# Kernel tuning notes

Measured on AMD Instinct MI355X. Metric: run time of the kernel, lower is better.

## Reference

```python
import jax, jax.numpy as jnp
import numpy as np

B, S, HID = 2, 4096, 1024
NH, HD = 16, 64
R = 2  # dilation_rate


def setup_inputs() -> dict:
    key = jax.random.key(0)
    ks = jax.random.split(key, 6)
    sc = 0.02
    return {
        "hidden_states": jax.random.normal(ks[0], (B, S, HID), jnp.float32),
        "Wq": jax.random.normal(ks[1], (HID, HID), jnp.float32) * sc,
        "Wk": jax.random.normal(ks[2], (HID, HID), jnp.float32) * sc,
        "Wv": jax.random.normal(ks[3], (HID, HID), jnp.float32) * sc,
        "Wo": jax.random.normal(ks[4], (HID, HID), jnp.float32) * sc,
        "bo": jnp.zeros((HID,), jnp.float32),
    }


def reference(hidden_states, Wq, Wk, Wv, Wo, bo):
    bsz, q_len, _ = hidden_states.shape
    # projections (torch Linear: y = x @ W.T)
    q = jnp.einsum('bsh,oh->bso', hidden_states, Wq).reshape(bsz, q_len, NH, HD).transpose(0, 2, 1, 3)
    k = jnp.einsum('bsh,oh->bso', hidden_states, Wk).reshape(bsz, q_len, NH, HD).transpose(0, 2, 1, 3)
    v = jnp.einsum('bsh,oh->bso', hidden_states, Wv).reshape(bsz, q_len, NH, HD).transpose(0, 2, 1, 3)
    # strided dilation gather (indices 0, R, 2R, ...)
    q = q[:, :, ::R, :]
    k = k[:, :, ::R, :]
    v = v[:, :, ::R, :]
    sd = q.shape[2]  # dilated length
    # SDPA with is_causal=True over the dilated subsequence
    scores = jnp.einsum('bhqd,bhkd->bhqk', q, k) / np.sqrt(HD).astype(np.float32)
    causal = jnp.tril(jnp.ones((sd, sd), bool))
    scores = jnp.where(causal, scores, jnp.finfo(scores.dtype).min)
    probs = jax.nn.softmax(scores, axis=-1)
    attn = jnp.einsum('bhqk,bhkd->bhqd', probs, v)  # [B, H, sd, HD]
    attn = attn.transpose(0, 2, 1, 3).reshape(bsz, sd, HID)
    # scatter back into zero-initialized full-length tensor
    full = jnp.zeros((bsz, q_len, HID), attn.dtype).at[:, ::R, :].set(attn)
    return jnp.einsum('bsh,oh->bso', full, Wo) + bo
```

## Files before the change

### kernel.cpp

```cpp
#include <hip/hip_runtime.h>
#include <cstdint>

typedef unsigned short u16;
typedef unsigned int u32;
typedef __attribute__((ext_vector_type(8))) short short8;
typedef __attribute__((ext_vector_type(4))) float f32x4;
typedef __attribute__((ext_vector_type(4))) unsigned short u16x4;

#define S_ 4096
#define SD 2048

__device__ __forceinline__ u16 f2bf(float f) {
  union { float f; u32 u; } v; v.f = f;
  u32 r = v.u + 0x7fffu + ((v.u >> 16) & 1u);
  return (u16)(r >> 16);
}
__device__ __forceinline__ float bf2f(u16 x) {
  union { u32 u; float f; } v; v.u = ((u32)x) << 16; return v.f;
}
#if __has_builtin(__builtin_amdgcn_cvt_pk_bf16_f32)
__device__ __forceinline__ u32 pkbf(float a, float b) {
  auto r = __builtin_amdgcn_cvt_pk_bf16_f32(a, b);
  u32 o; __builtin_memcpy(&o, &r, 4); return o;
}
#else
__device__ __forceinline__ u32 pkbf(float a, float b) {
  union { float f; u32 u; } ua, ub; ua.f = a; ub.f = b;
  return __builtin_amdgcn_perm(ub.u + 0x8000u, ua.u + 0x8000u, 0x07060302u);
}
#endif
__device__ __forceinline__ f32x4 mfma16(short8 a, short8 b, f32x4 c) {
  return __builtin_amdgcn_mfma_f32_16x16x32_bf16(a, b, c, 0, 0, 0);
}
__device__ __forceinline__ void async16(const void* g, void* l) {
  __builtin_amdgcn_global_load_lds((__attribute__((address_space(1))) void*)g,
                                   (__attribute__((address_space(3))) void*)l,
                                   16, 0, 0);
}

__global__ __launch_bounds__(256) void cast_all(const float* __restrict__ hs,
                                                const float* __restrict__ Wq,
                                                const float* __restrict__ Wk,
                                                const float* __restrict__ Wv,
                                                const float* __restrict__ Wo,
                                                u16* __restrict__ dstW,
                                                u16* __restrict__ dstX) {
  int bid = blockIdx.x;
  if (bid < 4096) {
    int gid = bid * 256 + threadIdx.x;
    int wsel = gid >> 18;
    int off  = (gid & 262143) * 4;
    const float* src = (wsel == 0) ? Wq : (wsel == 1) ? Wk : (wsel == 2) ? Wv : Wo;
    float scl = (wsel == 0) ? 0.18033688f : 1.0f;
    f32x4 v = *(const f32x4*)(src + off);
    u16x4 o; o.x = f2bf(v.x * scl); o.y = f2bf(v.y * scl);
    o.z = f2bf(v.z * scl); o.w = f2bf(v.w * scl);
    *(u16x4*)(dstW + (size_t)wsel * 1048576 + off) = o;
  } else {
    int gid = (bid - 4096) * 256 + threadIdx.x;
    int e = gid * 4;
    int m = e >> 10, col = e & 1023;
    int b = m >> 11, sm = m & 2047;
    const float* src = hs + ((size_t)(b * S_ + 2 * sm) << 10) + col;
    f32x4 v = *(const f32x4*)src;
    u16x4 o; o.x = f2bf(v.x); o.y = f2bf(v.y); o.z = f2bf(v.z); o.w = f2bf(v.w);
    *(u16x4*)(dstX + ((size_t)m << 10) + col) = o;
  }
}

template<int MODE>
__device__ __forceinline__ void gemm_body128_t(const u16* __restrict__ A,
                                               const u16* __restrict__ B,
                                               u16* __restrict__ C,
                                               int bm, int bn, char* lA, char* lB) {
  const int tid = threadIdx.x, lane = tid & 63, w = tid >> 6;
  const int quad = lane >> 4, l15 = lane & 15;
  const int wm = (w & 1) * 64, wn = (w >> 1) * 64;
  f32x4 acc[4][4] = {};

  auto stage = [&](int buf, int k0) {
#pragma unroll
    for (int i = 0; i < 2; i++) {
      int p = i * 256 + tid;
      int row = p >> 2, cp = p & 3;
      int c = cp ^ ((row ^ (row >> 2)) & 3);
      async16(A + (size_t)(bm + row) * 1024 + k0 + c * 8,
              lA + buf * 8192 + i * 4096 + w * 1024);
      async16(B + (size_t)(bn + row) * 1024 + k0 + c * 8,
              lB + buf * 8192 + i * 4096 + w * 1024);
    }
  };

  stage(0, 0);
#pragma unroll 1
  for (int kt = 0; kt < 32; kt++) {
    __syncthreads();
    if (kt + 1 < 32) stage((kt + 1) & 1, (kt + 1) * 32);
    const char* A_ = lA + (kt & 1) * 8192;
    const char* B_ = lB + (kt & 1) * 8192;
    short8 af[4], bf[4];
#pragma unroll
    for (int mi = 0; mi < 4; mi++) {
      int row = wm + mi * 16 + l15;
      af[mi] = *(const short8*)(A_ + (row * 4 + (quad ^ ((row ^ (row >> 2)) & 3))) * 16);
    }
#pragma unroll
    for (int ni = 0; ni < 4; ni++) {
      int row = wn + ni * 16 + l15;
      bf[ni] = *(const short8*)(B_ + (row * 4 + (quad ^ ((row ^ (row >> 2)) & 3))) * 16);
    }
#pragma unroll
    for (int mi = 0; mi < 4; mi++)
#pragma unroll
      for (int ni = 0; ni < 4; ni++)
        acc[mi][ni] = mfma16(af[mi], bf[ni], acc[mi][ni]);
  }

#pragma unroll
  for (int mi = 0; mi < 4; mi++)
#pragma unroll
    for (int ni = 0; ni < 4; ni++) {
      int m0 = bm + wm + mi * 16 + quad * 4;
      int n = bn + wn + ni * 16 + l15;
      size_t base;
      if (MODE == 0) {
        base = (size_t)m0 * 1024 + n;
      } else if (MODE == 1) {
        int bb = m0 >> 11, t = m0 & 2047, kb = t >> 6, key0 = t & 63;
        int d = n - 1024;
        int hh = d >> 6, dd = d & 63, ch = dd >> 3, e = dd & 7;
        base = ((size_t)(((bb * 16 + hh) * 32 + kb)) << 12)
             + (key0 >> 4) * 1024 + (ch >> 2) * 512 + (ch & 3) * 128
             + (key0 & 15) * 8 + e;
      } else {
        int hh = m0 >> 6, d0 = m0 & 63;
        int bb = n >> 11, t = n & 2047, kb = t >> 6, kk = t & 63;
        int kh = (kk & 32) | (((kk >> 2) & 3) << 3) | (((kk >> 4) & 1) << 2) | (kk & 3);
        int ch = kh >> 3, e = kh & 7;
        base = ((size_t)(((bb * 16 + hh) * 32 + kb)) << 12)
             + (d0 >> 4) * 1024 + (ch >> 2) * 512 + (ch & 3) * 128
             + (d0 & 15) * 8 + e;
      }
#pragma unroll
      for (int r = 0; r < 4; r++) {
        size_t off = (MODE == 0) ? base + (size_t)r * 1024 : base + (size_t)r * 8;
        C[off] = f2bf(acc[mi][ni][r]);
      }
    }
}

__global__ __launch_bounds__(256) void qkv_gemm(const u16* __restrict__ X,
                                                const u16* __restrict__ Wbf,
                                                u16* __restrict__ Qb,
                                                u16* __restrict__ Kp,
                                                u16* __restrict__ Vp) {
  __shared__ __align__(16) char lA[16384];
  __shared__ __align__(16) char lB[16384];
  int bid = blockIdx.x;
  if (bid < 512) {
    int bm = (bid >> 4) * 128, bn = (bid & 15) * 128;
    if (bn < 1024) gemm_body128_t<0>(X, Wbf, Qb, bm, bn, lA, lB);
    else           gemm_body128_t<1>(X, Wbf, Kp, bm, bn, lA, lB);
  } else {
    int b2 = bid - 512;
    gemm_body128_t<2>(Wbf + 2 * 1048576, X, Vp, (b2 >> 5) * 128, (b2 & 31) * 128, lA, lB);
  }
}

__global__ __launch_bounds__(256) void oproj(const u16* __restrict__ A,
                                             const u16* __restrict__ B,
                                             const float* __restrict__ bo,
                                             float* __restrict__ out) {
  __shared__ __align__(16) char lA[8192];
  __shared__ __align__(16) char lB[16384];
  const int tid = threadIdx.x, lane = tid & 63, w = tid >> 6;
  const int quad = lane >> 4, l15 = lane & 15;
  const int bm = blockIdx.y * 64, bn = blockIdx.x * 128;
  const int wm = (w & 1) * 32, wn = (w >> 1) * 64;
  f32x4 acc[2][4] = {};

  auto stage = [&](int buf, int k0) {
    {
      int row = tid >> 2, cp = tid & 3;
      int c = cp ^ ((row ^ (row >> 2)) & 3);
      async16(A + (size_t)(bm + row) * 1024 + k0 + c * 8, lA + buf * 4096 + w * 1024);
    }
#pragma unroll
    for (int i = 0; i < 2; i++) {
      int p = i * 256 + tid;
      int row = p >> 2, cp = p & 3;
      int c = cp ^ ((row ^ (row >> 2)) & 3);
      async16(B + (size_t)(bn + row) * 1024 + k0 + c * 8, lB + buf * 8192 + i * 4096 + w * 1024);
    }
  };

  stage(0, 0);
#pragma unroll 1
  for (int kt = 0; kt < 32; kt++) {
    __syncthreads();
    if (kt + 1 < 32) stage((kt + 1) & 1, (kt + 1) * 32);
    const char* A_ = lA + (kt & 1) * 4096;
    const char* B_ = lB + (kt & 1) * 8192;
    short8 af[2], bf[4];
#pragma unroll
    for (int mi = 0; mi < 2; mi++) {
      int row = wm + mi * 16 + l15;
      af[mi] = *(const short8*)(A_ + (row * 4 + (quad ^ ((row ^ (row >> 2)) & 3))) * 16);
    }
#pragma unroll
    for (int ni = 0; ni < 4; ni++) {
      int row = wn + ni * 16 + l15;
      bf[ni] = *(const short8*)(B_ + (row * 4 + (quad ^ ((row ^ (row >> 2)) & 3))) * 16);
    }
#pragma unroll
    for (int mi = 0; mi < 2; mi++)
#pragma unroll
      for (int ni = 0; ni < 4; ni++)
        acc[mi][ni] = mfma16(af[mi], bf[ni], acc[mi][ni]);
  }
#pragma unroll
  for (int mi = 0; mi < 2; mi++)
#pragma unroll
    for (int ni = 0; ni < 4; ni++) {
      int n = bn + wn + ni * 16 + l15;
      float bias = bo[n];
#pragma unroll
      for (int r = 0; r < 4; r++) {
        int m = bm + wm + mi * 16 + quad * 4 + r;
        int bb = m >> 11, sm = m & 2047;
        size_t grow = ((size_t)(bb * S_ + 2 * sm)) << 10;
        out[grow + n] = acc[mi][ni][r] + bias;
        out[grow + 1024 + n] = bias;
      }
    }
}

__global__ __launch_bounds__(256, 3) void attn11(const u16* __restrict__ Qb,
                                                 const u16* __restrict__ Kp,
                                                 const u16* __restrict__ Vp,
                                                 u16* __restrict__ O,
                                                 float* __restrict__ Op0,
                                                 u16* __restrict__ Op1,
                                                 float* __restrict__ lp) {
  const int tid = threadIdx.x, lane = tid & 63, w = tid >> 6;
  const int quad = lane >> 4, l15 = lane & 15;
  const int h = blockIdx.x, b = blockIdx.y;
  const int z = (int)blockIdx.z;
  int qt, chunk, c0, c1;
  if (z < 16) {
    qt = 15 - (z >> 1); chunk = z & 1;
    if (chunk == 0) { c0 = 0; c1 = qt; } else { c0 = qt + 1; c1 = 2 * qt + 1; }
  } else {
    qt = 23 - z; chunk = 0; c0 = 0; c1 = 2 * qt + 1;
  }
  const bool par = (z < 16);
  const int qb = qt * 128 + w * 32;
  const int qt2 = 2 * qt;

  short8 qf[2][2];
#pragma unroll
  for (int n = 0; n < 2; n++) {
    const u16* qp = Qb + (size_t)(b * SD + qb + n * 16 + l15) * 1024 + h * 64 + quad * 8;
    qf[n][0] = *(const short8*)qp;
    qf[n][1] = *(const short8*)(qp + 32);
  }

  const size_t bh = (size_t)(b * 16 + h) * 32;
  f32x4 oacc[2][4] = {};
  f32x4 l4v[2] = {};
  const f32x4 zf = {};

#pragma unroll 1
  for (int kt = c0; kt <= c1; kt++) {
    const u16* K_ = Kp + ((bh + kt) << 12);
    const u16* V_ = Vp + ((bh + kt) << 12);
    const bool diag = (kt >= qt2);

    short8 kf[4][2];
#pragma unroll
    for (int m = 0; m < 4; m++) {
      kf[m][0] = *(const short8*)(K_ + m * 1024 + lane * 8);
      kf[m][1] = *(const short8*)(K_ + m * 1024 + 512 + lane * 8);
    }
    f32x4 s[4][2];
#pragma unroll
    for (int m = 0; m < 4; m++)
#pragma unroll
      for (int n = 0; n < 2; n++) {
        f32x4 a = mfma16(kf[m][0], qf[n][0], zf);
        s[m][n] = mfma16(kf[m][1], qf[n][1], a);
      }
    short8 vf[4][2];
#pragma unroll
    for (int m = 0; m < 4; m++) {
      vf[m][0] = *(const short8*)(V_ + m * 1024 + lane * 8);
      vf[m][1] = *(const short8*)(V_ + m * 1024 + 512 + lane * 8);
    }
    u32 pw[2][8];
#pragma unroll
    for (int m = 0; m < 4; m++)
#pragma unroll
      for (int n = 0; n < 2; n++) {
        f32x4 a = s[m][n];
        if (diag) {
          int qrel = w * 32 + n * 16 + l15;
          int kd = (kt - qt2) * 64 + m * 16 + quad * 4;
#pragma unroll
          for (int r = 0; r < 4; r++)
            if (kd + r > qrel) a[r] = -1e30f;
        }
        f32x4 p;
#pragma unroll
        for (int r = 0; r < 4; r++) p[r] = exp2f(a[r]);
        l4v[n] += p;
        pw[n][m * 2]     = pkbf(p[0], p[1]);
        pw[n][m * 2 + 1] = pkbf(p[2], p[3]);
      }
    short8 pf[2][2];
#pragma unroll
    for (int n = 0; n < 2; n++) {
      __builtin_memcpy(&pf[n][0], &pw[n][0], 16);
      __builtin_memcpy(&pf[n][1], &pw[n][4], 16);
    }
#pragma unroll
    for (int m = 0; m < 4; m++)
#pragma unroll
      for (int n = 0; n < 2; n++) {
        oacc[n][m] = mfma16(vf[m][0], pf[n][0], oacc[n][m]);
        oacc[n][m] = mfma16(vf[m][1], pf[n][1], oacc[n][m]);
      }
  }

#pragma unroll
  for (int n = 0; n < 2; n++) {
    float l = (l4v[n][0] + l4v[n][1]) + (l4v[n][2] + l4v[n][3]);
    l += __shfl_xor(l, 16, 64);
    l += __shfl_xor(l, 32, 64);
    if (!par) {
      float inv = 1.0f / l;
      u16* op = O + (size_t)(b * SD + qb + n * 16 + l15) * 1024 + h * 64;
#pragma unroll
      for (int m = 0; m < 4; m++) {
        u16x4 ov;
#pragma unroll
        for (int r = 0; r < 4; r++) ov[r] = f2bf(oacc[n][m][r] * inv);
        *(u16x4*)(op + m * 16 + quad * 4) = ov;
      }
    } else {
      int rq = b * 1024 + (qb + n * 16 + l15 - 1024);
      if (chunk == 0) {
        float* p0 = Op0 + ((size_t)rq << 10) + h * 64 + quad * 4;
#pragma unroll
        for (int m = 0; m < 4; m++)
          *(f32x4*)(p0 + m * 16) = oacc[n][m];
      } else {
        u16* p1 = Op1 + ((size_t)rq << 10) + h * 64 + quad * 4;
#pragma unroll
        for (int m = 0; m < 4; m++) {
          u16x4 ov;
#pragma unroll
          for (int r = 0; r < 4; r++) ov[r] = f2bf(oacc[n][m][r]);
          *(u16x4*)(p1 + m * 16) = ov;
        }
      }
      if (quad == 0) lp[chunk * 32768 + rq * 16 + h] = l;
    }
  }
}

__global__ __launch_bounds__(256) void combine_po(const float* __restrict__ Op0,
                                                  const u16* __restrict__ Op1,
                                                  const float* __restrict__ lp,
                                                  u16* __restrict__ O) {
  int gid = blockIdx.x * 256 + threadIdx.x;
  int row = gid >> 8;
  int d0 = (gid & 255) * 4;
  int hh = d0 >> 6;
  float l = lp[row * 16 + hh] + lp[32768 + row * 16 + hh];
  float inv = 1.0f / l;
  f32x4 a = *(const f32x4*)(Op0 + ((size_t)row << 10) + d0);
  u16x4 b1 = *(const u16x4*)(Op1 + ((size_t)row << 10) + d0);
  int bb = row >> 10, qr = row & 1023;
  u16* op = O + ((size_t)(bb * SD + 1024 + qr) << 10) + d0;
  u16x4 o;
#pragma unroll
  for (int r = 0; r < 4; r++)
    o[r] = f2bf((a[r] + bf2f(b1[r])) * inv);
  *(u16x4*)op = o;
}

extern "C" void kernel_launch(void* const* d_in, const int* in_sizes, int n_in,
                              void* d_out, int out_size, void* d_ws, size_t ws_size,
                              hipStream_t stream) {
  (void)in_sizes; (void)n_in; (void)out_size; (void)ws_size;
  const float* hs = (const float*)d_in[0];
  const float* Wq = (const float*)d_in[1];
  const float* Wk = (const float*)d_in[2];
  const float* Wv = (const float*)d_in[3];
  const float* Wo = (const float*)d_in[4];
  const float* bo = (const float*)d_in[5];
  float* out = (float*)d_out;
  char* ws = (char*)d_ws;

  u16* Xbf = (u16*)ws;
  u16* Wbf = (u16*)(ws + (8u << 20));
  u16* Qb  = (u16*)(ws + (16u << 20));
  u16* Kp  = (u16*)(ws + (24u << 20));
  u16* Vp  = (u16*)(ws + (32u << 20));
  u16* Ob  = (u16*)(ws + (40u << 20));

  float* Op0 = (float*)ws;
  float* lp  = (float*)(ws + (8u << 20));
  u16*   Op1 = (u16*)(ws + (9u << 20));

  cast_all<<<8192, 256, 0, stream>>>(hs, Wq, Wk, Wv, Wo, Wbf, Xbf);
  qkv_gemm<<<768, 256, 0, stream>>>(Xbf, Wbf, Qb, Kp, Vp);
  attn11<<<dim3(16, 2, 24), 256, 0, stream>>>(Qb, Kp, Vp, Ob, Op0, Op1, lp);
  combine_po<<<2048, 256, 0, stream>>>(Op0, Op1, lp, Ob);
  oproj<<<dim3(8, 64), 256, 0, stream>>>(Ob, Wbf + 3 * 1048576, bo, out);
}
```

Baseline: 201.8 us.

## Split long causal attention rows into more KV chunks merged with atomics

Attention work is now split across 40 z-slices using a lookup table, which cuts the longer query tiles into up to four KV chunks. Partial outputs and row sums are accumulated in fp32 with atomicAdd into a workspace zeroed by a memset, and a simpler normalize kernel then writes the result. Occupancy is raised to 4 blocks per SM. The aim is better load balance and shorter tail latency, at the cost of atomic traffic, an extra memset, and a non-deterministic summation order.

```diff
diff --git a/kernel.cpp b/kernel.cpp
--- a/kernel.cpp
+++ b/kernel.cpp
@@ -15,9 +15,6 @@
   u32 r = v.u + 0x7fffu + ((v.u >> 16) & 1u);
   return (u16)(r >> 16);
 }
-__device__ __forceinline__ float bf2f(u16 x) {
-  union { u32 u; float f; } v; v.u = ((u32)x) << 16; return v.f;
-}
 #if __has_builtin(__builtin_amdgcn_cvt_pk_bf16_f32)
 __device__ __forceinline__ u32 pkbf(float a, float b) {
   auto r = __builtin_amdgcn_cvt_pk_bf16_f32(a, b);
@@ -37,6 +34,16 @@
                                    (__attribute__((address_space(3))) void*)l,
                                    16, 0, 0);
 }
+
+__device__ const signed char ZQT[40] = {15,15,15,15, 14,14,14,14, 13,13,13,13, 12,12,12,12,
+                                        11,11,11, 10,10,10, 9,9,9, 8,8,8,
+                                        7,7, 6,6, 5,5, 4,4, 3,2,1,0};
+__device__ const signed char ZC0[40] = {0,8,16,24, 0,8,16,23, 0,7,14,21, 0,7,14,20,
+                                        0,8,16, 0,8,15, 0,7,14, 0,6,12,
+                                        0,8, 0,7, 0,6, 0,5, 0,0,0,0};
+__device__ const signed char ZC1[40] = {7,15,23,31, 7,15,22,29, 6,13,20,27, 6,13,19,25,
+                                        7,15,23, 7,14,21, 6,13,19, 5,11,17,
+                                        7,15, 6,13, 5,11, 4,9, 7,5,3,1};
 
 __global__ __launch_bounds__(256) void cast_all(const float* __restrict__ hs,
                                                 const float* __restrict__ Wq,
@@ -235,25 +242,18 @@
     }
 }
 
-__global__ __launch_bounds__(256, 3) void attn11(const u16* __restrict__ Qb,
+__global__ __launch_bounds__(256, 4) void attn12(const u16* __restrict__ Qb,
                                                  const u16* __restrict__ Kp,
                                                  const u16* __restrict__ Vp,
                                                  u16* __restrict__ O,
-                                                 float* __restrict__ Op0,
-                                                 u16* __restrict__ Op1,
-                                                 float* __restrict__ lp) {
+                                                 float* __restrict__ Opart,
+                                                 float* __restrict__ lpart) {
   const int tid = threadIdx.x, lane = tid & 63, w = tid >> 6;
   const int quad = lane >> 4, l15 = lane & 15;
   const int h = blockIdx.x, b = blockIdx.y;
   const int z = (int)blockIdx.z;
-  int qt, chunk, c0, c1;
-  if (z < 16) {
-    qt = 15 - (z >> 1); chunk = z & 1;
-    if (chunk == 0) { c0 = 0; c1 = qt; } else { c0 = qt + 1; c1 = 2 * qt + 1; }
-  } else {
-    qt = 23 - z; chunk = 0; c0 = 0; c1 = 2 * qt + 1;
-  }
-  const bool par = (z < 16);
+  const int qt = ZQT[z], c0 = ZC0[z], c1 = ZC1[z];
+  const bool par = (z < 36);
   const int qb = qt * 128 + w * 32;
   const int qt2 = 2 * qt;
 
@@ -347,45 +347,33 @@
         *(u16x4*)(op + m * 16 + quad * 4) = ov;
       }
     } else {
-      int rq = b * 1024 + (qb + n * 16 + l15 - 1024);
-      if (chunk == 0) {
-        float* p0 = Op0 + ((size_t)rq << 10) + h * 64 + quad * 4;
-#pragma unroll
-        for (int m = 0; m < 4; m++)
-          *(f32x4*)(p0 + m * 16) = oacc[n][m];
-      } else {
-        u16* p1 = Op1 + ((size_t)rq << 10) + h * 64 + quad * 4;
-#pragma unroll
-        for (int m = 0; m < 4; m++) {
-          u16x4 ov;
-#pragma unroll
-          for (int r = 0; r < 4; r++) ov[r] = f2bf(oacc[n][m][r]);
-          *(u16x4*)(p1 + m * 16) = ov;
-        }
-      }
-      if (quad == 0) lp[chunk * 32768 + rq * 16 + h] = l;
-    }
-  }
-}
-
-__global__ __launch_bounds__(256) void combine_po(const float* __restrict__ Op0,
-                                                  const u16* __restrict__ Op1,
-                                                  const float* __restrict__ lp,
-                                                  u16* __restrict__ O) {
+      int rr = b * 1536 + (qb + n * 16 + l15 - 512);
+      float* p0 = Opart + ((size_t)rr << 10) + h * 64 + quad * 4;
+#pragma unroll
+      for (int m = 0; m < 4; m++)
+#pragma unroll
+        for (int r = 0; r < 4; r++)
+          atomicAdd(p0 + m * 16 + r, oacc[n][m][r]);
+      if (quad == 0) atomicAdd(&lpart[rr * 16 + h], l);
+    }
+  }
+}
+
+__global__ __launch_bounds__(256) void norm_po(const float* __restrict__ Opart,
+                                               const float* __restrict__ lpart,
+                                               u16* __restrict__ O) {
   int gid = blockIdx.x * 256 + threadIdx.x;
-  int row = gid >> 8;
-  int d0 = (gid & 255) * 4;
-  int hh = d0 >> 6;
-  float l = lp[row * 16 + hh] + lp[32768 + row * 16 + hh];
+  int e = gid * 4;
+  int row = e >> 10, d0 = e & 1023;
+  float l = lpart[row * 16 + (d0 >> 6)];
   float inv = 1.0f / l;
-  f32x4 a = *(const f32x4*)(Op0 + ((size_t)row << 10) + d0);
-  u16x4 b1 = *(const u16x4*)(Op1 + ((size_t)row << 10) + d0);
-  int bb = row >> 10, qr = row & 1023;
-  u16* op = O + ((size_t)(bb * SD + 1024 + qr) << 10) + d0;
+  f32x4 a = *(const f32x4*)(Opart + ((size_t)row << 10) + d0);
+  int bb = row >= 1536 ? 1 : 0;
+  int rr = row - bb * 1536;
+  u16* op = O + ((size_t)(bb * SD + 512 + rr) << 10) + d0;
   u16x4 o;
 #pragma unroll
-  for (int r = 0; r < 4; r++)
-    o[r] = f2bf((a[r] + bf2f(b1[r])) * inv);
+  for (int r = 0; r < 4; r++) o[r] = f2bf(a[r] * inv);
   *(u16x4*)op = o;
 }
 
@@ -409,13 +397,13 @@
   u16* Vp  = (u16*)(ws + (32u << 20));
   u16* Ob  = (u16*)(ws + (40u << 20));
 
-  float* Op0 = (float*)ws;
-  float* lp  = (float*)(ws + (8u << 20));
-  u16*   Op1 = (u16*)(ws + (9u << 20));
+  float* Opart = (float*)ws;
+  float* lpart = (float*)(ws + (12u << 20));
 
   cast_all<<<8192, 256, 0, stream>>>(hs, Wq, Wk, Wv, Wo, Wbf, Xbf);
   qkv_gemm<<<768, 256, 0, stream>>>(Xbf, Wbf, Qb, Kp, Vp);
-  attn11<<<dim3(16, 2, 24), 256, 0, stream>>>(Qb, Kp, Vp, Ob, Op0, Op1, lp);
-  combine_po<<<2048, 256, 0, stream>>>(Op0, Op1, lp, Ob);
+  hipMemsetAsync(ws, 0, (12u << 20) + (1u << 18), stream);
+  attn12<<<dim3(16, 2, 40), 256, 0, stream>>>(Qb, Kp, Vp, Ob, Opart, lpart);
+  norm_po<<<3072, 256, 0, stream>>>(Opart, lpart, Ob);
   oproj<<<dim3(8, 64), 256, 0, stream>>>(Ob, Wbf + 3 * 1048576, bo, out);
 }
```

Result: slower. 333.0 us (+65.0%).

## Rebalance causal attention split-K with table-driven 36-way tile partition

Applied to the files above, without the earlier changes.

Replaces the 24-slice z-dimension work split with a 36-entry lookup table. The table assigns query tiles and key-tile ranges so each block does roughly equal causal work, and long query tiles are split into up to three chunks. Partial outputs are stored as bf16 rather than fp32, and one chunk writes its partial directly into the output buffer. The combine kernel is rewritten to sum up to three partials. Launch bounds are raised to 5 blocks per CU for more occupancy, at the risk of register spilling and extra rounding from bf16 partials.

```diff
diff --git a/kernel.cpp b/kernel.cpp
--- a/kernel.cpp
+++ b/kernel.cpp
@@ -37,6 +37,11 @@
                                    (__attribute__((address_space(3))) void*)l,
                                    16, 0, 0);
 }
+
+__device__ const signed char ZQT[36] = {15,15,15,14,14,14,13,13,13,12,12,12,11,11,11,10, 7, 7, 3,10,10, 9, 9, 6, 6, 9, 8, 8, 8, 5, 5, 2, 4, 4, 1, 0};
+__device__ const signed char ZC0[36] = { 0,11,22, 0,10,20, 0,10,19, 0, 9,18, 0, 8,16, 0, 0, 8, 0, 8,15, 0, 7, 0, 7,14, 0, 6,12, 0, 6, 0, 0, 5, 0, 0};
+__device__ const signed char ZC1[36] = {10,21,31, 9,19,29, 9,18,27, 8,17,25, 7,15,23, 7, 7,15, 7,14,21, 6,13, 6,13,19, 5,11,17, 5,11, 5, 4, 9, 3, 1};
+__device__ const signed char ZDS[36] = { 0, 1, 2, 0, 1, 2, 0, 1, 2, 0, 1, 2, 0, 1, 2, 0, 0, 2, 3, 1, 2, 0, 1, 0, 2, 2, 0, 1, 2, 0, 2, 3, 0, 2, 3, 3};
 
 __global__ __launch_bounds__(256) void cast_all(const float* __restrict__ hs,
                                                 const float* __restrict__ Wq,
@@ -235,25 +240,20 @@
     }
 }
 
-__global__ __launch_bounds__(256, 3) void attn11(const u16* __restrict__ Qb,
+__global__ __launch_bounds__(256, 5) void attn13(const u16* __restrict__ Qb,
                                                  const u16* __restrict__ Kp,
                                                  const u16* __restrict__ Vp,
                                                  u16* __restrict__ O,
-                                                 float* __restrict__ Op0,
-                                                 u16* __restrict__ Op1,
-                                                 float* __restrict__ lp) {
+                                                 u16* __restrict__ P0,
+                                                 u16* __restrict__ P1,
+                                                 float* __restrict__ lpA,
+                                                 float* __restrict__ lpB,
+                                                 float* __restrict__ lpC) {
   const int tid = threadIdx.x, lane = tid & 63, w = tid >> 6;
   const int quad = lane >> 4, l15 = lane & 15;
   const int h = blockIdx.x, b = blockIdx.y;
   const int z = (int)blockIdx.z;
-  int qt, chunk, c0, c1;
-  if (z < 16) {
-    qt = 15 - (z >> 1); chunk = z & 1;
-    if (chunk == 0) { c0 = 0; c1 = qt; } else { c0 = qt + 1; c1 = 2 * qt + 1; }
-  } else {
-    qt = 23 - z; chunk = 0; c0 = 0; c1 = 2 * qt + 1;
-  }
-  const bool par = (z < 16);
+  const int qt = ZQT[z], c0 = ZC0[z], c1 = ZC1[z], dest = ZDS[z];
   const int qb = qt * 128 + w * 32;
   const int qt2 = 2 * qt;
 
@@ -336,9 +336,10 @@
     float l = (l4v[n][0] + l4v[n][1]) + (l4v[n][2] + l4v[n][3]);
     l += __shfl_xor(l, 16, 64);
     l += __shfl_xor(l, 32, 64);
-    if (!par) {
+    const int q = qb + n * 16 + l15;
+    if (dest == 3) {
       float inv = 1.0f / l;
-      u16* op = O + (size_t)(b * SD + qb + n * 16 + l15) * 1024 + h * 64;
+      u16* op = O + (size_t)(b * SD + q) * 1024 + h * 64;
 #pragma unroll
       for (int m = 0; m < 4; m++) {
         u16x4 ov;
@@ -347,45 +348,61 @@
         *(u16x4*)(op + m * 16 + quad * 4) = ov;
       }
     } else {
-      int rq = b * 1024 + (qb + n * 16 + l15 - 1024);
-      if (chunk == 0) {
-        float* p0 = Op0 + ((size_t)rq << 10) + h * 64 + quad * 4;
-#pragma unroll
-        for (int m = 0; m < 4; m++)
-          *(f32x4*)(p0 + m * 16) = oacc[n][m];
+      u16* pdst;
+      if (dest == 0) {
+        int rq = b * 1536 + (q - 512);
+        pdst = P0 + ((size_t)rq << 10) + h * 64 + quad * 4;
+        if (quad == 0) lpA[rq * 16 + h] = l;
+      } else if (dest == 1) {
+        int rq = b * 1024 + (q - 1024);
+        pdst = P1 + ((size_t)rq << 10) + h * 64 + quad * 4;
+        if (quad == 0) lpB[rq * 16 + h] = l;
       } else {
-        u16* p1 = Op1 + ((size_t)rq << 10) + h * 64 + quad * 4;
-#pragma unroll
-        for (int m = 0; m < 4; m++) {
-          u16x4 ov;
-#pragma unroll
-          for (int r = 0; r < 4; r++) ov[r] = f2bf(oacc[n][m][r]);
-          *(u16x4*)(p1 + m * 16) = ov;
-        }
-      }
-      if (quad == 0) lp[chunk * 32768 + rq * 16 + h] = l;
-    }
-  }
-}
-
-__global__ __launch_bounds__(256) void combine_po(const float* __restrict__ Op0,
-                                                  const u16* __restrict__ Op1,
-                                                  const float* __restrict__ lp,
-                                                  u16* __restrict__ O) {
+        pdst = O + (size_t)(b * SD + q) * 1024 + h * 64 + quad * 4;
+        int rq = b * 1536 + (q - 512);
+        if (quad == 0) lpC[rq * 16 + h] = l;
+      }
+#pragma unroll
+      for (int m = 0; m < 4; m++) {
+        u16x4 ov;
+#pragma unroll
+        for (int r = 0; r < 4; r++) ov[r] = f2bf(oacc[n][m][r]);
+        *(u16x4*)(pdst + m * 16) = ov;
+      }
+    }
+  }
+}
+
+__global__ __launch_bounds__(256) void norm2(const u16* __restrict__ P0,
+                                             const u16* __restrict__ P1,
+                                             const float* __restrict__ lpA,
+                                             const float* __restrict__ lpB,
+                                             const float* __restrict__ lpC,
+                                             u16* __restrict__ O) {
   int gid = blockIdx.x * 256 + threadIdx.x;
   int row = gid >> 8;
   int d0 = (gid & 255) * 4;
   int hh = d0 >> 6;
-  float l = lp[row * 16 + hh] + lp[32768 + row * 16 + hh];
+  int b = row >= 1536 ? 1 : 0;
+  int qr = row - b * 1536;
+  float l = lpA[row * 16 + hh] + lpC[row * 16 + hh];
+  u16x4 a0 = *(const u16x4*)(P0 + ((size_t)row << 10) + d0);
+  u16* op = O + ((size_t)(b * SD + 512 + qr) << 10) + d0;
+  u16x4 ar = *(const u16x4*)op;
+  f32x4 acc;
+#pragma unroll
+  for (int r = 0; r < 4; r++) acc[r] = bf2f(a0[r]) + bf2f(ar[r]);
+  if (qr >= 512) {
+    int r1 = b * 1024 + (qr - 512);
+    l += lpB[r1 * 16 + hh];
+    u16x4 a1 = *(const u16x4*)(P1 + ((size_t)r1 << 10) + d0);
+#pragma unroll
+    for (int r = 0; r < 4; r++) acc[r] += bf2f(a1[r]);
+  }
   float inv = 1.0f / l;
-  f32x4 a = *(const f32x4*)(Op0 + ((size_t)row << 10) + d0);
-  u16x4 b1 = *(const u16x4*)(Op1 + ((size_t)row << 10) + d0);
-  int bb = row >> 10, qr = row & 1023;
-  u16* op = O + ((size_t)(bb * SD + 1024 + qr) << 10) + d0;
   u16x4 o;
 #pragma unroll
-  for (int r = 0; r < 4; r++)
-    o[r] = f2bf((a[r] + bf2f(b1[r])) * inv);
+  for (int r = 0; r < 4; r++) o[r] = f2bf(acc[r] * inv);
   *(u16x4*)op = o;
 }
 
@@ -409,13 +426,15 @@
   u16* Vp  = (u16*)(ws + (32u << 20));
   u16* Ob  = (u16*)(ws + (40u << 20));
 
-  float* Op0 = (float*)ws;
-  float* lp  = (float*)(ws + (8u << 20));
-  u16*   Op1 = (u16*)(ws + (9u << 20));
+  u16*   P0  = (u16*)ws;
+  u16*   P1  = (u16*)(ws + (6u << 20));
+  float* lpA = (float*)(ws + (10u << 20));
+  float* lpB = (float*)(ws + (10u << 20) + (256u << 10));
+  float* lpC = (float*)(ws + (10u << 20) + (512u << 10));
 
   cast_all<<<8192, 256, 0, stream>>>(hs, Wq, Wk, Wv, Wo, Wbf, Xbf);
   qkv_gemm<<<768, 256, 0, stream>>>(Xbf, Wbf, Qb, Kp, Vp);
-  attn11<<<dim3(16, 2, 24), 256, 0, stream>>>(Qb, Kp, Vp, Ob, Op0, Op1, lp);
-  combine_po<<<2048, 256, 0, stream>>>(Op0, Op1, lp, Ob);
+  attn13<<<dim3(16, 2, 36), 256, 0, stream>>>(Qb, Kp, Vp, Ob, P0, P1, lpA, lpB, lpC);
+  norm2<<<3072, 256, 0, stream>>>(P0, P1, lpA, lpB, lpC, Ob);
   oproj<<<dim3(8, 64), 256, 0, stream>>>(Ob, Wbf + 3 * 1048576, bo, out);
 }
```

Result: slower. 298.3 us (+47.8%).
